# Optimization experiments

Hardware: AMD Instinct MI355X
Metric: run time of the kernel (lower is better)

## Reference

```python
import jax, jax.numpy as jnp
import numpy as np

V = 32          # number_variables
DEG = 12        # degree
ORDER = 3       # spline_order (cubic)
N_BASIS = DEG + ORDER - 1  # 14, rows of params
LO, HI = -15.0, 15.0       # polynomial_range[:, 0]
EPS = 1e-6


def make_knots():
    dist = (HI - LO) / (DEG - 1)
    k = DEG + 2 * ORDER
    return jnp.linspace(LO - ORDER * dist, HI + ORDER * dist, k, dtype=jnp.float32)


def bspline_basis(x, knots, order):
    # x: [N, P] -> basis: [N, P, N_BASIS] via Cox-de Boor recursion (Naive_Basis)
    xk = x[..., None]
    b = ((xk >= knots[:-1]) & (xk < knots[1:])).astype(x.dtype)  # degree-0, [N,P,K-1]
    t = knots
    for k in range(1, order + 1):
        left = (xk - t[:-(k + 1)]) / (t[k:-1] - t[:-(k + 1)])
        right = (t[k + 1:] - xk) / (t[k + 1:] - t[1:-k])
        b = left * b[..., :-1] + right * b[..., 1:]
    return b  # [N, P, K-1-order] == [N, P, N_BASIS]


def setup_inputs() -> dict:
    key = jax.random.key(0)
    k1, k2 = jax.random.split(key)
    num_lambdas = V * (V - 1) // 2  # 496
    inp = jax.random.normal(k1, (16384, V), dtype=jnp.float32)
    log_d = jnp.zeros((16384, V), dtype=jnp.float32)
    params = 0.001 * jnp.ones((N_BASIS, num_lambdas), dtype=jnp.float32)
    return {"input": inp, "log_d": log_d, "params": params}


def reference(input, log_d, params):
    n = input.shape[0]
    knots = make_knots()
    rows, cols = np.tril_indices(V, -1)  # matches torch.tril_indices(V, V, offset=-1)
    rows = jnp.asarray(rows); cols = jnp.asarray(cols)
    # clamp into half-open spline support for valid degree-0 basis
    x = jnp.clip(input, LO, HI - EPS)
    xs = x[:, cols]                                  # [N, P] per-pair covariate values
    basis = bspline_basis(xs, knots, ORDER)          # [N, P, N_BASIS]
    lam = jnp.einsum('npk,kp->np', basis, params)    # [N, P] lambda values
    # lower-triangular lambda matrix: identity + strict lower entries
    lm = jnp.broadcast_to(jnp.eye(V, dtype=input.dtype), (n, V, V))
    lm = lm.at[:, rows, cols].set(lam)
    out = jnp.einsum('nvc,nc->nv', lm, input)        # bmm(lambda_matrix, input)
    # ridge penalties on spline coefficients (penalize_towards=0)
    d2 = jnp.diff(params, n=2, axis=0)
    d1 = jnp.diff(params, n=1, axis=0)
    second_pen = jnp.sum(d2 ** 2)
    first_pen = jnp.sum(d1 ** 2)
    param_pen = jnp.sum(params ** 2)
    return out, lm, second_pen, first_pen, param_pen
```

## Files before the change

kernel.cpp:

```cpp
#include <hip/hip_runtime.h>

#define VDIM   32
#define NPAIR  496
#define NBASIS 14

__global__ __launch_bounds__(256) void Decorrelation_35270271435435_kernel(
    const float* __restrict__ input,
    const float* __restrict__ params,
    float* __restrict__ out,
    float* __restrict__ lm,
    float* __restrict__ pens)
{
    const int n   = blockIdx.x;
    const int tid = threadIdx.x;

    __shared__ float xin[VDIM];
    __shared__ float wgt[VDIM][4];
    __shared__ int   ibase[VDIM];

    if (tid < VDIM) {
        float xi = input[n * VDIM + tid];
        xin[tid] = xi;
        const float LOf  = -15.0f;
        const float HIf  = 15.0f;
        const float EPSf = 1e-6f;
        const float dist = 30.0f / 11.0f;
        const float invd = 11.0f / 30.0f;
        const float t0   = LOf - 3.0f * dist;
        float x = fminf(fmaxf(xi, LOf), HIf - EPSf);
        float u = (x - t0) * invd;
        int   i = (int)floorf(u);
        i = min(13, max(3, i));
        float uu  = u - (float)i;
        float om  = 1.0f - uu;
        float uu2 = uu * uu, uu3 = uu2 * uu;
        const float sixth = 1.0f / 6.0f;
        wgt[tid][0] = om * om * om * sixth;
        wgt[tid][1] = (3.0f * uu3 - 6.0f * uu2 + 4.0f) * sixth;
        wgt[tid][2] = (-3.0f * uu3 + 3.0f * uu2 + 3.0f * uu + 1.0f) * sixth;
        wgt[tid][3] = uu3 * sixth;
        ibase[tid]  = (i - 3) * NPAIR;
    }
    __syncthreads();

    const int v  = tid >> 3;
    const int c0 = (tid & 7) << 2;
    float vals[4];
    float partial = 0.0f;
    #pragma unroll
    for (int j = 0; j < 4; ++j) {
        const int c = c0 + j;
        float val;
        if (c == v) {
            val = 1.0f;
        } else if (c < v) {
            const int p = (v * (v - 1)) / 2 + c;
            const int b = ibase[c] + p;
            val = wgt[c][0] * params[b]
                + wgt[c][1] * params[b + NPAIR]
                + wgt[c][2] * params[b + 2 * NPAIR]
                + wgt[c][3] * params[b + 3 * NPAIR];
        } else {
            val = 0.0f;
        }
        vals[j] = val;
        partial += val * xin[c];
    }
    float4 f4 = make_float4(vals[0], vals[1], vals[2], vals[3]);
    *(float4*)(lm + (size_t)n * (VDIM * VDIM) + tid * 4) = f4;

    partial += __shfl_down(partial, 4, 8);
    partial += __shfl_down(partial, 2, 8);
    partial += __shfl_down(partial, 1, 8);
    if ((tid & 7) == 0) out[n * VDIM + v] = partial;

    if (blockIdx.x == 0) {
        float s2 = 0.0f, s1 = 0.0f, sp = 0.0f;
        const int NP = NBASIS * NPAIR;
        for (int idx = tid; idx < NP; idx += 256) {
            const float a = params[idx];
            sp += a * a;
            if (idx < NP - NPAIR) {
                const float b = params[idx + NPAIR];
                const float d1 = b - a;
                s1 += d1 * d1;
                if (idx < NP - 2 * NPAIR) {
                    const float c = params[idx + 2 * NPAIR];
                    const float d2 = c - 2.0f * b + a;
                    s2 += d2 * d2;
                }
            }
        }
        #pragma unroll
        for (int off = 32; off > 0; off >>= 1) {
            s2 += __shfl_down(s2, off);
            s1 += __shfl_down(s1, off);
            sp += __shfl_down(sp, off);
        }
        __shared__ float wsum[3][4];
        const int lane = tid & 63, wid = tid >> 6;
        if (lane == 0) { wsum[0][wid] = s2; wsum[1][wid] = s1; wsum[2][wid] = sp; }
        __syncthreads();
        if (tid == 0) {
            pens[0] = wsum[0][0] + wsum[0][1] + wsum[0][2] + wsum[0][3];
            pens[1] = wsum[1][0] + wsum[1][1] + wsum[1][2] + wsum[1][3];
            pens[2] = wsum[2][0] + wsum[2][1] + wsum[2][2] + wsum[2][3];
        }
    }
}

extern "C" void kernel_launch(void* const* d_in, const int* in_sizes, int n_in,
                              void* d_out, int out_size, void* d_ws, size_t ws_size,
                              hipStream_t stream) {
    const float* input  = (const float*)d_in[0];
    const float* params = (const float*)d_in[2];
    const int N = in_sizes[0] / VDIM;

    float* out  = (float*)d_out;
    float* lm   = out + (size_t)N * VDIM;
    float* pens = lm + (size_t)N * VDIM * VDIM;

    Decorrelation_35270271435435_kernel<<<N, 256, 0, stream>>>(input, params, out, lm, pens);
}
```

Measured before the change: 105.1 us.

## Process 16 rows per block with params staged in shared memory

Each block now handles 16 samples instead of one. It copies the whole 14x496 parameter table into LDS once per block and computes the spline weights for all 16 rows cooperatively. The large lambda-matrix output is written with nontemporal stores, and the penalty reduction reads from LDS. The aim is to amortise block launch and setup and to cut repeated global/L2 gathers of params. The cost is about 30KB of LDS per block, which lowers occupancy, plus an extra staging load per block.

```diff
diff --git a/kernel.cpp b/kernel.cpp
--- a/kernel.cpp
+++ b/kernel.cpp
@@ -3,89 +3,116 @@
 #define VDIM   32
 #define NPAIR  496
 #define NBASIS 14
+#define NPARAM (NBASIS * NPAIR)
+#define ROWS   16
+
+typedef float f32x4 __attribute__((ext_vector_type(4)));
 
 __global__ __launch_bounds__(256) void Decorrelation_35270271435435_kernel(
     const float* __restrict__ input,
     const float* __restrict__ params,
     float* __restrict__ out,
     float* __restrict__ lm,
-    float* __restrict__ pens)
+    float* __restrict__ pens,
+    int N)
 {
-    const int n   = blockIdx.x;
+    __shared__ float sp[NPARAM];
+    __shared__ float xin[ROWS][VDIM];
+    __shared__ float wgt[4][ROWS][VDIM];
+    __shared__ int   ib [ROWS][VDIM];
+
     const int tid = threadIdx.x;
+    const int n0  = blockIdx.x * ROWS;
 
-    __shared__ float xin[VDIM];
-    __shared__ float wgt[VDIM][4];
-    __shared__ int   ibase[VDIM];
+    {
+        const f32x4* p4 = (const f32x4*)params;
+        f32x4*       s4 = (f32x4*)sp;
+        for (int i = tid; i < NPARAM / 4; i += 256) s4[i] = p4[i];
+    }
 
-    if (tid < VDIM) {
-        float xi = input[n * VDIM + tid];
-        xin[tid] = xi;
-        const float LOf  = -15.0f;
-        const float HIf  = 15.0f;
-        const float EPSf = 1e-6f;
+    #pragma unroll
+    for (int it = 0; it < 2; ++it) {
+        const int item = tid + it * 256;
+        const int r = item >> 5, c = item & 31;
+        const int n = n0 + r;
+        const float xi = (n < N) ? input[n * VDIM + c] : 0.0f;
+        xin[r][c] = xi;
         const float dist = 30.0f / 11.0f;
         const float invd = 11.0f / 30.0f;
-        const float t0   = LOf - 3.0f * dist;
-        float x = fminf(fmaxf(xi, LOf), HIf - EPSf);
+        const float t0   = -15.0f - 3.0f * dist;
+        float x = fminf(fmaxf(xi, -15.0f), 15.0f - 1e-6f);
         float u = (x - t0) * invd;
         int   i = (int)floorf(u);
         i = min(13, max(3, i));
-        float uu  = u - (float)i;
-        float om  = 1.0f - uu;
-        float uu2 = uu * uu, uu3 = uu2 * uu;
+        const float uu  = u - (float)i;
+        const float om  = 1.0f - uu;
+        const float uu2 = uu * uu, uu3 = uu2 * uu;
         const float sixth = 1.0f / 6.0f;
-        wgt[tid][0] = om * om * om * sixth;
-        wgt[tid][1] = (3.0f * uu3 - 6.0f * uu2 + 4.0f) * sixth;
-        wgt[tid][2] = (-3.0f * uu3 + 3.0f * uu2 + 3.0f * uu + 1.0f) * sixth;
-        wgt[tid][3] = uu3 * sixth;
-        ibase[tid]  = (i - 3) * NPAIR;
+        wgt[0][r][c] = om * om * om * sixth;
+        wgt[1][r][c] = (3.0f * uu3 - 6.0f * uu2 + 4.0f) * sixth;
+        wgt[2][r][c] = (-3.0f * uu3 + 3.0f * uu2 + 3.0f * uu + 1.0f) * sixth;
+        wgt[3][r][c] = uu3 * sixth;
+        ib[r][c] = (i - 3) * NPAIR;
     }
     __syncthreads();
 
     const int v  = tid >> 3;
     const int c0 = (tid & 7) << 2;
-    float vals[4];
-    float partial = 0.0f;
+    int  pidx[4];
+    bool low[4], dia[4];
     #pragma unroll
     for (int j = 0; j < 4; ++j) {
         const int c = c0 + j;
-        float val;
-        if (c == v) {
-            val = 1.0f;
-        } else if (c < v) {
-            const int p = (v * (v - 1)) / 2 + c;
-            const int b = ibase[c] + p;
-            val = wgt[c][0] * params[b]
-                + wgt[c][1] * params[b + NPAIR]
-                + wgt[c][2] * params[b + 2 * NPAIR]
-                + wgt[c][3] * params[b + 3 * NPAIR];
-        } else {
-            val = 0.0f;
+        low[j]  = (c < v);
+        dia[j]  = (c == v);
+        pidx[j] = (v * (v - 1)) / 2 + c;
+    }
+
+    float* lmp = lm + (size_t)n0 * (VDIM * VDIM) + tid * 4;
+
+    for (int r = 0; r < ROWS; ++r, lmp += VDIM * VDIM) {
+        const int n = n0 + r;
+        if (n >= N) break;
+        float vals[4];
+        float partial = 0.0f;
+        #pragma unroll
+        for (int j = 0; j < 4; ++j) {
+            const int c = c0 + j;
+            float val;
+            if (dia[j]) {
+                val = 1.0f;
+            } else if (low[j]) {
+                const int b = ib[r][c] + pidx[j];
+                val = wgt[0][r][c] * sp[b]
+                    + wgt[1][r][c] * sp[b + NPAIR]
+                    + wgt[2][r][c] * sp[b + 2 * NPAIR]
+                    + wgt[3][r][c] * sp[b + 3 * NPAIR];
+            } else {
+                val = 0.0f;
+            }
+            vals[j] = val;
+            partial += val * xin[r][c];
         }
-        vals[j] = val;
-        partial += val * xin[c];
+        f32x4 f4 = { vals[0], vals[1], vals[2], vals[3] };
+        __builtin_nontemporal_store(f4, (f32x4*)lmp);
+
+        partial += __shfl_down(partial, 4, 8);
+        partial += __shfl_down(partial, 2, 8);
+        partial += __shfl_down(partial, 1, 8);
+        if ((tid & 7) == 0) out[n * VDIM + v] = partial;
     }
-    float4 f4 = make_float4(vals[0], vals[1], vals[2], vals[3]);
-    *(float4*)(lm + (size_t)n * (VDIM * VDIM) + tid * 4) = f4;
-
-    partial += __shfl_down(partial, 4, 8);
-    partial += __shfl_down(partial, 2, 8);
-    partial += __shfl_down(partial, 1, 8);
-    if ((tid & 7) == 0) out[n * VDIM + v] = partial;
 
     if (blockIdx.x == 0) {
-        float s2 = 0.0f, s1 = 0.0f, sp = 0.0f;
-        const int NP = NBASIS * NPAIR;
-        for (int idx = tid; idx < NP; idx += 256) {
-            const float a = params[idx];
-            sp += a * a;
-            if (idx < NP - NPAIR) {
-                const float b = params[idx + NPAIR];
+        float s2 = 0.0f, s1 = 0.0f, spn = 0.0f;
+        for (int idx = tid; idx < NPARAM; idx += 256) {
+            const float a = sp[idx];
+            spn += a * a;
+            if (idx < NPARAM - NPAIR) {
+                const float b = sp[idx + NPAIR];
                 const float d1 = b - a;
                 s1 += d1 * d1;
-                if (idx < NP - 2 * NPAIR) {
-                    const float c = params[idx + 2 * NPAIR];
+                if (idx < NPARAM - 2 * NPAIR) {
+                    const float c = sp[idx + 2 * NPAIR];
                     const float d2 = c - 2.0f * b + a;
                     s2 += d2 * d2;
                 }
@@ -93,13 +120,13 @@
         }
         #pragma unroll
         for (int off = 32; off > 0; off >>= 1) {
-            s2 += __shfl_down(s2, off);
-            s1 += __shfl_down(s1, off);
-            sp += __shfl_down(sp, off);
+            s2  += __shfl_down(s2, off);
+            s1  += __shfl_down(s1, off);
+            spn += __shfl_down(spn, off);
         }
         __shared__ float wsum[3][4];
         const int lane = tid & 63, wid = tid >> 6;
-        if (lane == 0) { wsum[0][wid] = s2; wsum[1][wid] = s1; wsum[2][wid] = sp; }
+        if (lane == 0) { wsum[0][wid] = s2; wsum[1][wid] = s1; wsum[2][wid] = spn; }
         __syncthreads();
         if (tid == 0) {
             pens[0] = wsum[0][0] + wsum[0][1] + wsum[0][2] + wsum[0][3];
@@ -120,5 +147,7 @@
     float* lm   = out + (size_t)N * VDIM;
     float* pens = lm + (size_t)N * VDIM * VDIM;
 
-    Decorrelation_35270271435435_kernel<<<N, 256, 0, stream>>>(input, params, out, lm, pens);
+    const int nb = (N + ROWS - 1) / ROWS;
+    Decorrelation_35270271435435_kernel<<<nb, 256, 0, stream>>>(
+        input, params, out, lm, pens, N);
 }
```

Measured after the change: 93.99 us. 1.12x faster.
